# Optimization experiments

Hardware: AMD Instinct MI355X
Metric: run time of the kernel (lower is better)

Reference implementation:

```python
import jax, jax.numpy as jnp
import numpy as np


def setup_inputs() -> dict:
    key = jax.random.key(0)
    k1, k2 = jax.random.split(key)
    B, N, D = 32, 8192, 64
    x = jax.random.normal(k1, (B, N, D), dtype=jnp.float32)
    y = jax.random.normal(k2, (B, D, N), dtype=jnp.float32)
    return {"x": x, "y": y}


def reference(x, y):
    # Original: full cdist [B,N,N], mean over batch, take diagonal.
    # Only matched pairs (i,i) survive, so compute them directly —
    # mathematically identical output and gradients.
    y_t = jnp.transpose(y, (0, 2, 1))          # [B, N, D]
    diff = x - y_t                             # [B, N, D]
    pair_dist = jnp.sqrt(jnp.sum(diff * diff, axis=-1))  # [B, N]
    dist_diag = jnp.mean(pair_dist, axis=0)    # [N] == diag(mean_b cdist)
    dist_diag = dist_diag.at[1:3].multiply(1.5)
    loss = jnp.mean(dist_diag)
    return loss
```

## Files before the change

kernel.cpp:

```cpp
#include <hip/hip_runtime.h>


constexpr int B  = 32;
constexpr int N  = 8192;
constexpr int D  = 64;
constexpr int QD = D / 4;
constexpr int NPB = 64;

__global__ __launch_bounds__(256, 4) void euclid_loss_kernel(
    const float* __restrict__ x,
    const float* __restrict__ y,
    float* __restrict__ out)
{
    const int tid  = threadIdx.x;
    const int wave = tid >> 6;
    const int lane = tid & 63;
    const int n    = blockIdx.x * NPB + lane;
    const int b    = blockIdx.y;

    const float* xp = x + ((size_t)b * N + n) * D + wave * QD;
    const float* yp = y + (size_t)b * D * N + (size_t)(wave * QD) * N + n;

    float4 xv[4];
#pragma unroll
    for (int j = 0; j < 4; ++j)
        xv[j] = *reinterpret_cast<const float4*>(xp + 4 * j);

    float yv[QD];
#pragma unroll
    for (int d = 0; d < QD; ++d)
        yv[d] = yp[(size_t)d * N];

    asm volatile("" ::: "memory");

    float acc = 0.0f;
#pragma unroll
    for (int j = 0; j < 4; ++j) {
        const float d0 = xv[j].x - yv[4 * j + 0];
        const float d1 = xv[j].y - yv[4 * j + 1];
        const float d2 = xv[j].z - yv[4 * j + 2];
        const float d3 = xv[j].w - yv[4 * j + 3];
        acc += d0 * d0 + d1 * d1 + d2 * d2 + d3 * d3;
    }

    __shared__ float part[4][NPB];
    part[wave][lane] = acc;
    __syncthreads();

    if (tid < NPB) {
        const float s = part[0][tid] + part[1][tid] + part[2][tid] + part[3][tid];
        const float w = (n == 1 || n == 2) ? 1.5f : 1.0f;
        float v = w * __builtin_sqrtf(s);
#pragma unroll
        for (int off = 32; off > 0; off >>= 1) v += __shfl_down(v, off, 64);
        if (tid == 0)
            atomicAdd(out, v * (1.0f / (float)(B * N)));
    }
}

extern "C" void kernel_launch(void* const* d_in, const int* in_sizes, int n_in,
                              void* d_out, int out_size, void* d_ws, size_t ws_size,
                              hipStream_t stream) {
    const float* x = (const float*)d_in[0];
    const float* y = (const float*)d_in[1];
    float* out = (float*)d_out;

    hipMemsetAsync(out, 0, sizeof(float), stream);

    dim3 grid(N / NPB, B);
    euclid_loss_kernel<<<grid, 256, 0, stream>>>(x, y, out);
}
```

Baseline: 165.4 us.

## Stage x and y tiles through LDS using direct global-to-LDS loads

Replaces the per-thread register loads with buffer global_load_lds instructions that copy a 64x64 x tile and a 64x64 y tile straight into shared memory, then computes the differences from LDS using a rotated index to avoid bank conflicts. The goal is fully coalesced, wide global reads for x (the old per-lane x loads were strided by row) and less register pressure from holding values in flight. In exchange it uses 32KB of LDS per block, which caps occupancy, and adds extra barriers and LDS traffic. The launch_bounds occupancy hint is also dropped.

```diff
diff --git a/kernel.cpp b/kernel.cpp
--- a/kernel.cpp
+++ b/kernel.cpp
@@ -4,51 +4,58 @@
 constexpr int B  = 32;
 constexpr int N  = 8192;
 constexpr int D  = 64;
-constexpr int QD = D / 4;
-constexpr int NPB = 64;
+constexpr int TN = 64;
 
-__global__ __launch_bounds__(256, 4) void euclid_loss_kernel(
+#define GLD_LDS(gp, lp, sz)                                                              \
+    __builtin_amdgcn_global_load_lds(                                                    \
+        (const __attribute__((address_space(1))) void*)(gp),                             \
+        (__attribute__((address_space(3))) void*)(lp), (sz), 0, 0)
+
+__global__ __launch_bounds__(256) void euclid_loss_kernel(
     const float* __restrict__ x,
     const float* __restrict__ y,
     float* __restrict__ out)
 {
+    __shared__ float x_s[TN * D];
+    __shared__ float y_s[D * TN];
+
     const int tid  = threadIdx.x;
     const int wave = tid >> 6;
     const int lane = tid & 63;
-    const int n    = blockIdx.x * NPB + lane;
+    const int n0   = blockIdx.x * TN;
     const int b    = blockIdx.y;
 
-    const float* xp = x + ((size_t)b * N + n) * D + wave * QD;
-    const float* yp = y + (size_t)b * D * N + (size_t)(wave * QD) * N + n;
+    const float* xg = x + ((size_t)b * N + n0) * D;
+    const float* yg = y + (size_t)b * D * N + n0;
 
-    float4 xv[4];
 #pragma unroll
-    for (int j = 0; j < 4; ++j)
-        xv[j] = *reinterpret_cast<const float4*>(xp + 4 * j);
+    for (int j = 0; j < 4; ++j) {
+        const int c = wave * 4 + j;
+        GLD_LDS(xg + c * 256 + lane * 4, x_s + c * 256, 16);
+    }
+#pragma unroll
+    for (int j = 0; j < 16; ++j) {
+        const int d = wave * 16 + j;
+        GLD_LDS(yg + (size_t)d * N + lane, y_s + d * TN, 4);
+    }
 
-    float yv[QD];
-#pragma unroll
-    for (int d = 0; d < QD; ++d)
-        yv[d] = yp[(size_t)d * N];
-
-    asm volatile("" ::: "memory");
+    __syncthreads();
 
     float acc = 0.0f;
 #pragma unroll
-    for (int j = 0; j < 4; ++j) {
-        const float d0 = xv[j].x - yv[4 * j + 0];
-        const float d1 = xv[j].y - yv[4 * j + 1];
-        const float d2 = xv[j].z - yv[4 * j + 2];
-        const float d3 = xv[j].w - yv[4 * j + 3];
-        acc += d0 * d0 + d1 * d1 + d2 * d2 + d3 * d3;
+    for (int s = 0; s < 16; ++s) {
+        const int d  = wave * 16 + ((lane + s) & 15);
+        const float df = x_s[lane * D + d] - y_s[d * TN + lane];
+        acc += df * df;
     }
 
-    __shared__ float part[4][NPB];
-    part[wave][lane] = acc;
+    __syncthreads();
+    x_s[wave * TN + lane] = acc;
     __syncthreads();
 
-    if (tid < NPB) {
-        const float s = part[0][tid] + part[1][tid] + part[2][tid] + part[3][tid];
+    if (tid < TN) {
+        const float s = x_s[tid] + x_s[TN + tid] + x_s[2 * TN + tid] + x_s[3 * TN + tid];
+        const int   n = n0 + tid;
         const float w = (n == 1 || n == 2) ? 1.5f : 1.0f;
         float v = w * __builtin_sqrtf(s);
 #pragma unroll
@@ -67,6 +74,6 @@
 
     hipMemsetAsync(out, 0, sizeof(float), stream);
 
-    dim3 grid(N / NPB, B);
+    dim3 grid(N / TN, B);
     euclid_loss_kernel<<<grid, 256, 0, stream>>>(x, y, out);
 }
```

Measured after the change: 168.4 us. About the same (+1.8%).
